# Performance work log

Hardware: AMD Instinct MI355X
Metric: run time of the kernel (lower is better)

Reference implementation:

```python
import jax, jax.numpy as jnp
import numpy as np
from jax import lax

B, S, H, W = 64, 256, 512, 512


def _lstm_cell(x_t, h, c, Wih, Whh, bih, bhh):
    # PyTorch LSTMCell gate order: i, f, g, o
    g = x_t @ Wih.T + h @ Whh.T + bih + bhh  # [B, 4H]
    i, f, gg, o = jnp.split(g, 4, axis=-1)
    c_new = jax.nn.sigmoid(f) * c + jax.nn.sigmoid(i) * jnp.tanh(gg)
    h_new = jax.nn.sigmoid(o) * jnp.tanh(c_new)
    return h_new, c_new


def setup_inputs() -> dict:
    key = jax.random.key(0)
    ks = jax.random.split(key, 12)
    bnd = 1.0 / np.sqrt(H)
    u = lambda k, shape, b: jax.random.uniform(k, shape, jnp.float32, -b, b)
    return {
        "x": jax.random.normal(ks[0], (B, S, S), jnp.float32),
        "enc_Wih": u(ks[1], (4 * H, S), bnd),
        "enc_Whh": u(ks[2], (4 * H, H), bnd),
        "enc_bih": u(ks[3], (4 * H,), bnd),
        "enc_bhh": u(ks[4], (4 * H,), bnd),
        "dec_Wih": u(ks[5], (4 * H, S), bnd),
        "dec_Whh": u(ks[6], (4 * H, H), bnd),
        "dec_bih": u(ks[7], (4 * H,), bnd),
        "dec_bhh": u(ks[8], (4 * H,), bnd),
        "w1": u(ks[9], (W, H), 1.0 / np.sqrt(H)),
        "w2": u(ks[10], (W, H), 1.0 / np.sqrt(H)),
        "vt": u(ks[11], (W,), 1.0 / np.sqrt(W)),
    }


def reference(x, enc_Wih, enc_Whh, enc_bih, enc_bhh,
              dec_Wih, dec_Whh, dec_bih, dec_bhh, w1, w2, vt):
    xs = x.transpose(1, 0, 2)  # [S, B, S] time-major

    # ---- encoder LSTM (zero initial state, PyTorch default) ----
    def enc_step(carry, x_t):
        h, c = carry
        h, c = _lstm_cell(x_t, h, c, enc_Wih, enc_Whh, enc_bih, enc_bhh)
        return (h, c), h

    h0 = jnp.zeros((B, H), x.dtype)
    (hT, cT), enc_out = lax.scan(enc_step, (h0, h0), xs)  # enc_out: [S, B, H]

    # loop-invariant W1 projection of encoder outputs
    e1 = jnp.einsum('sbh,wh->sbw', enc_out, w1)  # [S, B, W]

    # ---- decoder: hidden updates each step; cell stays at cT (faithful to source) ----
    def dec_step(h, x_t):
        h_new, _ = _lstm_cell(x_t, h, cT, dec_Wih, dec_Whh, dec_bih, dec_bhh)
        att = jnp.tanh(e1 + (h_new @ w2.T)[None, :, :])   # [S, B, W]
        scores = jnp.einsum('sbw,w->sb', att, vt)          # [S, B]
        lp = jax.nn.log_softmax(scores.T, axis=-1)         # [B, S]
        return h_new, lp

    _, probs = lax.scan(dec_step, hT, xs)  # [S_dec, B, S]
    return probs.transpose(1, 0, 2)        # [B, S_dec, S]
```

## Files before the change

kernel.cpp:

```cpp
#include <hip/hip_runtime.h>
#include <cmath>

__device__ __forceinline__ float sigm(float x) { return 1.0f / (1.0f + __expf(-x)); }

__global__ __launch_bounds__(256) void transpose_w(const float* __restrict__ in,
                                                   float* __restrict__ outT, int K) {
  __shared__ float tile[32][33];
  int tx = threadIdx.x & 31, ty = threadIdx.x >> 5;
  int k0 = blockIdx.x * 32;
  int j0 = blockIdx.y * 32;
#pragma unroll
  for (int i = 0; i < 32; i += 8)
    tile[ty + i][tx] = in[(size_t)(j0 + ty + i) * K + k0 + tx];
  __syncthreads();
#pragma unroll
  for (int i = 0; i < 32; i += 8)
    outT[(size_t)(k0 + ty + i) * 2048 + j0 + tx] = tile[tx][ty + i];
}

__device__ __forceinline__ void gemv_j(const float4* __restrict__ A4,
                                       const float4* __restrict__ W4, int j, int kqx,
                                       int kq, int jlo, int jhi, int b0, int b1,
                                       float (&o0)[8], float (&o1)[8]) {
  int qa = (j << 3) + kqx;
  float4 a04 = A4[b0 * 192 + qa];
  float4 a14 = A4[b1 * 192 + qa];
  int wr = ((j << 3) + kq) << 2;
  float a0v[4] = {a04.x, a04.y, a04.z, a04.w};
  float a1v[4] = {a14.x, a14.y, a14.z, a14.w};
#pragma unroll
  for (int i = 0; i < 4; ++i) {
    float4 wlo = W4[(wr + i) * 8 + jlo];
    float4 whi = W4[(wr + i) * 8 + jhi];
    o0[0] = fmaf(a0v[i], wlo.x, o0[0]);
    o0[1] = fmaf(a0v[i], wlo.y, o0[1]);
    o0[2] = fmaf(a0v[i], wlo.z, o0[2]);
    o0[3] = fmaf(a0v[i], wlo.w, o0[3]);
    o0[4] = fmaf(a0v[i], whi.x, o0[4]);
    o0[5] = fmaf(a0v[i], whi.y, o0[5]);
    o0[6] = fmaf(a0v[i], whi.z, o0[6]);
    o0[7] = fmaf(a0v[i], whi.w, o0[7]);
    o1[0] = fmaf(a1v[i], wlo.x, o1[0]);
    o1[1] = fmaf(a1v[i], wlo.y, o1[1]);
    o1[2] = fmaf(a1v[i], wlo.z, o1[2]);
    o1[3] = fmaf(a1v[i], wlo.w, o1[3]);
    o1[4] = fmaf(a1v[i], whi.x, o1[4]);
    o1[5] = fmaf(a1v[i], whi.y, o1[5]);
    o1[6] = fmaf(a1v[i], whi.z, o1[6]);
    o1[7] = fmaf(a1v[i], whi.w, o1[7]);
  }
}

__global__ __launch_bounds__(256, 1) void lstm_chain(
    const float* __restrict__ WT, const float* __restrict__ x,
    const float* __restrict__ bih, const float* __restrict__ bhh,
    float* __restrict__ HBUF,
    float* __restrict__ Cst,
    unsigned int* __restrict__ flg,
    int is_enc) {
  extern __shared__ float lds[];
  float4* W4 = (float4*)lds;
  float4* A4 = (float4*)(lds + 24576);
  float* gates = lds + 24576 + 12288;
  const int bg = blockIdx.x >> 6, ng = blockIdx.x & 63;
  const int tid = threadIdx.x;
  unsigned int* myflag = flg + (size_t)(bg * 64 + ng) * 32;
  unsigned int* dom = flg + (size_t)bg * 64 * 32;

#pragma unroll
  for (int r = 0; r < 24; ++r) {
    int idx = tid + 256 * r;
    int k = idx >> 3, j = idx & 7;
    float4 v =
        *(const float4*)(WT + (size_t)k * 2048 + (j >> 1) * 512 + ng * 8 + (j & 1) * 4);
    W4[k * 8 + (j ^ ((k >> 2) & 7))] = v;
  }
  float bi_i = 0.f, bi_f = 0.f, bi_g = 0.f, bi_o = 0.f, creg = 0.f;
  if (tid < 128) {
    int b = tid >> 3, n8 = tid & 7;
    int n_g = ng * 8 + n8;
    bi_i = bih[n_g] + bhh[n_g];
    bi_f = bih[512 + n_g] + bhh[512 + n_g];
    bi_g = bih[1024 + n_g] + bhh[1024 + n_g];
    bi_o = bih[1536 + n_g] + bhh[1536 + n_g];
    if (!is_enc) creg = Cst[(size_t)(bg * 16 + b) * 512 + n_g];
  }
#pragma unroll
  for (int r = 0; r < 8; ++r) {
    int idx = tid + 256 * r;
    int b = idx >> 7, q = idx & 127;
    float4 v;
    if (is_enc)
      v = make_float4(0.f, 0.f, 0.f, 0.f);
    else
      v = *(const float4*)(HBUF + ((size_t)(255 * 64) + bg * 16 + b) * 512 + 4 * q);
    A4[b * 192 + (q ^ ((b >> 1) & 7))] = v;
  }
#pragma unroll
  for (int r = 0; r < 4; ++r) {
    int idx = tid + 256 * r;
    int b = idx >> 6, q = idx & 63;
    float4 v = *(const float4*)(x + ((size_t)(bg * 16 + b) * 256 + 0) * 256 + 4 * q);
    A4[b * 192 + ((128 + q) ^ ((b >> 1) & 7))] = v;
  }
  __syncthreads();

  const int w = tid >> 6;
  const int lane = tid & 63;
  const int kq = lane >> 3, b8 = lane & 7;
  const int b0 = 2 * b8, b1 = b0 + 1;
  const int jlo = (2 * w) ^ kq, jhi = (2 * w + 1) ^ kq;
  const int kqx = kq ^ b8;

  for (int t = 0; t < 256; ++t) {
    float acc0[8], acc1[8];
#pragma unroll
    for (int g = 0; g < 8; ++g) { acc0[g] = 0.f; acc1[g] = 0.f; }
#pragma unroll 2
    for (int j = 0; j < 24; ++j)
      gemv_j(A4, W4, j, kqx, kq, jlo, jhi, b0, b1, acc0, acc1);
#pragma unroll
    for (int d = 8; d <= 32; d <<= 1) {
#pragma unroll
      for (int g = 0; g < 8; ++g) {
        acc0[g] += __shfl_xor(acc0[g], d, 64);
        acc1[g] += __shfl_xor(acc1[g], d, 64);
      }
    }
    if (kq == 0) {
#pragma unroll
      for (int g = 0; g < 8; ++g) {
        gates[b0 * 40 + w * 8 + g] = acc0[g];
        gates[b1 * 40 + w * 8 + g] = acc1[g];
      }
    }
    __syncthreads();
    if (tid < 128) {
      int b = tid >> 3, n8 = tid & 7;
      float pi = gates[b * 40 + n8] + bi_i;
      float pf = gates[b * 40 + 8 + n8] + bi_f;
      float pg = gates[b * 40 + 16 + n8] + bi_g;
      float po = gates[b * 40 + 24 + n8] + bi_o;
      float ig = sigm(pi), fg = sigm(pf), gg = tanhf(pg), og = sigm(po);
      float cn = fmaf(fg, creg, ig * gg);
      if (is_enc) creg = cn;
      float hn = og * tanhf(cn);
      float* hp = HBUF + ((size_t)t * 64 + bg * 16 + b) * 512 + ng * 8 + n8;
      __hip_atomic_store(hp, hn, __ATOMIC_RELAXED, __HIP_MEMORY_SCOPE_AGENT);
      if (is_enc && t == 255) Cst[(size_t)(bg * 16 + b) * 512 + ng * 8 + n8] = cn;
    }
    if (t == 255) break;
    asm volatile("s_waitcnt vmcnt(0)" ::: "memory");
    __syncthreads();
    if (tid == 0)
      __hip_atomic_store(myflag, (unsigned)(t + 1), __ATOMIC_RELAXED,
                         __HIP_MEMORY_SCOPE_AGENT);
    asm volatile("" ::: "memory");
#pragma unroll
    for (int r = 0; r < 4; ++r) {
      int idx = tid + 256 * r;
      int b = idx >> 6, q = idx & 63;
      float4 v =
          *(const float4*)(x + ((size_t)(bg * 16 + b) * 256 + (t + 1)) * 256 + 4 * q);
      A4[b * 192 + ((128 + q) ^ ((b >> 1) & 7))] = v;
    }
    if (tid < 64) {
      const unsigned tgt = (unsigned)(t + 1);
      unsigned int* fp = dom + (size_t)tid * 32;
      while (true) {
        unsigned v = __hip_atomic_load(fp, __ATOMIC_RELAXED, __HIP_MEMORY_SCOPE_AGENT);
        if (__all((int)(v >= tgt))) break;
        __builtin_amdgcn_s_sleep(1);
      }
    }
    __syncthreads();
    const float4* hb = (const float4*)(HBUF + (size_t)t * 64 * 512);
#pragma unroll
    for (int r = 0; r < 8; ++r) {
      int idx = tid + 256 * r;
      int b = idx >> 7, q = idx & 127;
      float4 v = hb[(size_t)(bg * 16 + b) * 128 + q];
      A4[b * 192 + (q ^ ((b >> 1) & 7))] = v;
    }
    __syncthreads();
  }
}

__global__ __launch_bounds__(256) void gemm_fp32(const float* __restrict__ A,
                                                 const float* __restrict__ W,
                                                 float* __restrict__ C, int N, int K) {
  __shared__ float As[16 * 132];
  __shared__ float Ws[16 * 132];
  int tid = threadIdx.x;
  int n0 = blockIdx.x * 128, m0 = blockIdx.y * 128;
  int row = tid >> 1;
  int kbase = (tid & 1) * 8;
  const float* ap = A + (size_t)(m0 + row) * K;
  const float* wp = W + (size_t)(n0 + row) * K;
  int ty = tid >> 4, tx = tid & 15;
  float acc[8][8];
#pragma unroll
  for (int i = 0; i < 8; ++i)
#pragma unroll
    for (int j = 0; j < 8; ++j) acc[i][j] = 0.f;

  for (int kt = 0; kt < K; kt += 16) {
    float4 va0 = *(const float4*)(ap + kt + kbase);
    float4 va1 = *(const float4*)(ap + kt + kbase + 4);
    float4 vw0 = *(const float4*)(wp + kt + kbase);
    float4 vw1 = *(const float4*)(wp + kt + kbase + 4);
    __syncthreads();
    As[(kbase + 0) * 132 + row] = va0.x;
    As[(kbase + 1) * 132 + row] = va0.y;
    As[(kbase + 2) * 132 + row] = va0.z;
    As[(kbase + 3) * 132 + row] = va0.w;
    As[(kbase + 4) * 132 + row] = va1.x;
    As[(kbase + 5) * 132 + row] = va1.y;
    As[(kbase + 6) * 132 + row] = va1.z;
    As[(kbase + 7) * 132 + row] = va1.w;
    Ws[(kbase + 0) * 132 + row] = vw0.x;
    Ws[(kbase + 1) * 132 + row] = vw0.y;
    Ws[(kbase + 2) * 132 + row] = vw0.z;
    Ws[(kbase + 3) * 132 + row] = vw0.w;
    Ws[(kbase + 4) * 132 + row] = vw1.x;
    Ws[(kbase + 5) * 132 + row] = vw1.y;
    Ws[(kbase + 6) * 132 + row] = vw1.z;
    Ws[(kbase + 7) * 132 + row] = vw1.w;
    __syncthreads();
#pragma unroll
    for (int kk = 0; kk < 16; ++kk) {
      float4 a0 = *(const float4*)&As[kk * 132 + ty * 8];
      float4 a1 = *(const float4*)&As[kk * 132 + ty * 8 + 4];
      float4 w0 = *(const float4*)&Ws[kk * 132 + tx * 8];
      float4 w1 = *(const float4*)&Ws[kk * 132 + tx * 8 + 4];
      float av[8] = {a0.x, a0.y, a0.z, a0.w, a1.x, a1.y, a1.z, a1.w};
      float wv[8] = {w0.x, w0.y, w0.z, w0.w, w1.x, w1.y, w1.z, w1.w};
#pragma unroll
      for (int i = 0; i < 8; ++i)
#pragma unroll
        for (int j = 0; j < 8; ++j) acc[i][j] = fmaf(av[i], wv[j], acc[i][j]);
    }
  }
#pragma unroll
  for (int i = 0; i < 8; ++i) {
    float* cp = C + (size_t)(m0 + ty * 8 + i) * N + n0 + tx * 8;
    *(float4*)cp = make_float4(acc[i][0], acc[i][1], acc[i][2], acc[i][3]);
    *(float4*)(cp + 4) = make_float4(acc[i][4], acc[i][5], acc[i][6], acc[i][7]);
  }
}

__global__ __launch_bounds__(256) void scorer(const float* __restrict__ E1,
                                              const float* __restrict__ H2,
                                              const float* __restrict__ vt,
                                              float* __restrict__ out) {
  extern __shared__ float smem[];
  float* e1s = smem;
  float* h2s = smem + 8256;
  int tid = threadIdx.x;
  int sx = blockIdx.x;
  int b = blockIdx.y;
#pragma unroll
  for (int j = 0; j < 8; ++j) {
    int idx = tid + 256 * j;
    int r = idx >> 7, c4 = idx & 127;
    float4 v = *(const float4*)(E1 + ((size_t)(sx * 16 + r) * 64 + b) * 512 + c4 * 4);
    *(float4*)&e1s[r * 516 + c4 * 4] = v;
  }
  int tl = tid >> 4, sl = tid & 15;
  for (int tt = 0; tt < 16; ++tt) {
    __syncthreads();
#pragma unroll
    for (int j = 0; j < 8; ++j) {
      int idx = tid + 256 * j;
      int r = idx >> 7, c4 = idx & 127;
      float4 v = *(const float4*)(H2 + ((size_t)(tt * 16 + r) * 64 + b) * 512 + c4 * 4);
      *(float4*)&h2s[r * 516 + c4 * 4] = v;
    }
    __syncthreads();
    float acc = 0.f;
    const float* ep = &e1s[sl * 516];
    const float* hp = &h2s[tl * 516];
#pragma unroll 8
    for (int w4 = 0; w4 < 128; ++w4) {
      float4 a = *(const float4*)(ep + w4 * 4);
      float4 h = *(const float4*)(hp + w4 * 4);
      float4 vv = *(const float4*)(vt + w4 * 4);
      float x0 = a.x + h.x, x1 = a.y + h.y, x2 = a.z + h.z, x3 = a.w + h.w;
      float t0 = fmaf(-2.f, __builtin_amdgcn_rcpf(__expf(x0 + x0) + 1.f), 1.f);
      float t1 = fmaf(-2.f, __builtin_amdgcn_rcpf(__expf(x1 + x1) + 1.f), 1.f);
      float t2 = fmaf(-2.f, __builtin_amdgcn_rcpf(__expf(x2 + x2) + 1.f), 1.f);
      float t3 = fmaf(-2.f, __builtin_amdgcn_rcpf(__expf(x3 + x3) + 1.f), 1.f);
      acc = fmaf(t0, vv.x, acc);
      acc = fmaf(t1, vv.y, acc);
      acc = fmaf(t2, vv.z, acc);
      acc = fmaf(t3, vv.w, acc);
    }
    out[((size_t)b * 256 + tt * 16 + tl) * 256 + sx * 16 + sl] = acc;
  }
}

__global__ __launch_bounds__(256) void logsoftmax_kernel(float* __restrict__ out) {
  __shared__ float red[256];
  int tid = threadIdx.x;
  float* row = out + (size_t)blockIdx.x * 256;
  float v = row[tid];
  red[tid] = v;
  __syncthreads();
  for (int off = 128; off > 0; off >>= 1) {
    if (tid < off) red[tid] = fmaxf(red[tid], red[tid + off]);
    __syncthreads();
  }
  float mx = red[0];
  __syncthreads();
  red[tid] = __expf(v - mx);
  __syncthreads();
  for (int off = 128; off > 0; off >>= 1) {
    if (tid < off) red[tid] += red[tid + off];
    __syncthreads();
  }
  float lse = logf(red[0]);
  row[tid] = v - mx - lse;
}

extern "C" void kernel_launch(void* const* d_in, const int* in_sizes, int n_in,
                              void* d_out, int out_size, void* d_ws, size_t ws_size,
                              hipStream_t stream) {
  (void)in_sizes; (void)n_in; (void)out_size; (void)ws_size;
  const float* x = (const float*)d_in[0];
  const float* eWih = (const float*)d_in[1];
  const float* eWhh = (const float*)d_in[2];
  const float* ebih = (const float*)d_in[3];
  const float* ebhh = (const float*)d_in[4];
  const float* dWih = (const float*)d_in[5];
  const float* dWhh = (const float*)d_in[6];
  const float* dbih = (const float*)d_in[7];
  const float* dbhh = (const float*)d_in[8];
  const float* w1 = (const float*)d_in[9];
  const float* w2 = (const float*)d_in[10];
  const float* vt = (const float*)d_in[11];
  float* out = (float*)d_out;
  float* ws = (float*)d_ws;

  float* E1 = ws;
  float* H2 = E1 + 8388608ull;
  float* HBUF = H2 + 8388608ull;
  float* WTe = HBUF + 8388608ull;
  float* WTd = WTe + 1572864ull;
  float* Cst = WTd + 1572864ull;
  unsigned int* FLG = (unsigned int*)(Cst + 32768ull);

  const unsigned ldsB = (24576 + 12288 + 640) * 4;
  const unsigned scorerLds = 2 * 16 * 516 * 4;

  hipMemsetAsync(FLG, 0, 16384 * sizeof(unsigned int), stream);
  transpose_w<<<dim3(16, 64), 256, 0, stream>>>(eWhh, WTe, 512);
  transpose_w<<<dim3(8, 64), 256, 0, stream>>>(eWih, WTe + 512 * 2048, 256);
  transpose_w<<<dim3(16, 64), 256, 0, stream>>>(dWhh, WTd, 512);
  transpose_w<<<dim3(8, 64), 256, 0, stream>>>(dWih, WTd + 512 * 2048, 256);

  {
    const float* a0 = WTe; const float* a1 = x; const float* a2 = ebih;
    const float* a3 = ebhh; float* a4 = HBUF; float* a5 = Cst;
    unsigned int* a6 = FLG; int a7 = 1;
    void* args[] = {&a0, &a1, &a2, &a3, &a4, &a5, &a6, &a7};
    hipLaunchCooperativeKernel((const void*)lstm_chain, dim3(256), dim3(256), args,
                               ldsB, stream);
  }
  gemm_fp32<<<dim3(4, 128), 256, 0, stream>>>(HBUF, w1, E1, 512, 512);
  {
    const float* a0 = WTd; const float* a1 = x; const float* a2 = dbih;
    const float* a3 = dbhh; float* a4 = HBUF; float* a5 = Cst;
    unsigned int* a6 = FLG + 8192; int a7 = 0;
    void* args[] = {&a0, &a1, &a2, &a3, &a4, &a5, &a6, &a7};
    hipLaunchCooperativeKernel((const void*)lstm_chain, dim3(256), dim3(256), args,
                               ldsB, stream);
  }
  gemm_fp32<<<dim3(4, 128), 256, 0, stream>>>(HBUF, w2, H2, 512, 512);
  scorer<<<dim3(16, 64), 256, scorerLds, stream>>>(E1, H2, vt, out);
  logsoftmax_kernel<<<16384, 256, 0, stream>>>(out);
}
```

Before: 4.029 ms.

## Double LSTM block threads, split flag signaling, and spread scorer over time chunks

The recurrent LSTM kernel now runs 512 threads per block, with each wavefront computing one gate for 8 batch rows, which halves the per-thread serial GEMV work in each step. The block-wide barrier before polling is replaced: two wavefronts each publish their own flag, one wavefront polls the peer flags and then releases the others through an LDS variable, so the whole block no longer waits on a barrier before polling. The scorer grid gains a z dimension so each block handles 2 time tiles instead of 16, giving more parallelism at the cost of reloading E1 in every block. Risks are the more intricate synchronisation protocol and higher register and occupancy pressure.

```diff
diff --git a/kernel.cpp b/kernel.cpp
--- a/kernel.cpp
+++ b/kernel.cpp
@@ -18,40 +18,7 @@
     outT[(size_t)(k0 + ty + i) * 2048 + j0 + tx] = tile[tx][ty + i];
 }
 
-__device__ __forceinline__ void gemv_j(const float4* __restrict__ A4,
-                                       const float4* __restrict__ W4, int j, int kqx,
-                                       int kq, int jlo, int jhi, int b0, int b1,
-                                       float (&o0)[8], float (&o1)[8]) {
-  int qa = (j << 3) + kqx;
-  float4 a04 = A4[b0 * 192 + qa];
-  float4 a14 = A4[b1 * 192 + qa];
-  int wr = ((j << 3) + kq) << 2;
-  float a0v[4] = {a04.x, a04.y, a04.z, a04.w};
-  float a1v[4] = {a14.x, a14.y, a14.z, a14.w};
-#pragma unroll
-  for (int i = 0; i < 4; ++i) {
-    float4 wlo = W4[(wr + i) * 8 + jlo];
-    float4 whi = W4[(wr + i) * 8 + jhi];
-    o0[0] = fmaf(a0v[i], wlo.x, o0[0]);
-    o0[1] = fmaf(a0v[i], wlo.y, o0[1]);
-    o0[2] = fmaf(a0v[i], wlo.z, o0[2]);
-    o0[3] = fmaf(a0v[i], wlo.w, o0[3]);
-    o0[4] = fmaf(a0v[i], whi.x, o0[4]);
-    o0[5] = fmaf(a0v[i], whi.y, o0[5]);
-    o0[6] = fmaf(a0v[i], whi.z, o0[6]);
-    o0[7] = fmaf(a0v[i], whi.w, o0[7]);
-    o1[0] = fmaf(a1v[i], wlo.x, o1[0]);
-    o1[1] = fmaf(a1v[i], wlo.y, o1[1]);
-    o1[2] = fmaf(a1v[i], wlo.z, o1[2]);
-    o1[3] = fmaf(a1v[i], wlo.w, o1[3]);
-    o1[4] = fmaf(a1v[i], whi.x, o1[4]);
-    o1[5] = fmaf(a1v[i], whi.y, o1[5]);
-    o1[6] = fmaf(a1v[i], whi.z, o1[6]);
-    o1[7] = fmaf(a1v[i], whi.w, o1[7]);
-  }
-}
-
-__global__ __launch_bounds__(256, 1) void lstm_chain(
+__global__ __launch_bounds__(512, 1) void lstm_chain(
     const float* __restrict__ WT, const float* __restrict__ x,
     const float* __restrict__ bih, const float* __restrict__ bhh,
     float* __restrict__ HBUF,
@@ -62,14 +29,16 @@
   float4* W4 = (float4*)lds;
   float4* A4 = (float4*)(lds + 24576);
   float* gates = lds + 24576 + 12288;
+  unsigned int* ldsrel = (unsigned int*)(lds + 24576 + 12288 + 640);
   const int bg = blockIdx.x >> 6, ng = blockIdx.x & 63;
   const int tid = threadIdx.x;
-  unsigned int* myflag = flg + (size_t)(bg * 64 + ng) * 32;
-  unsigned int* dom = flg + (size_t)bg * 64 * 32;
-
-#pragma unroll
-  for (int r = 0; r < 24; ++r) {
-    int idx = tid + 256 * r;
+  unsigned int* fl0 = flg + ((size_t)(bg * 64 + ng) * 2 + 0) * 32;
+  unsigned int* dmn = flg + (size_t)bg * 4096;
+  if (tid == 0) *ldsrel = 0u;
+
+#pragma unroll
+  for (int r = 0; r < 12; ++r) {
+    int idx = tid + 512 * r;
     int k = idx >> 3, j = idx & 7;
     float4 v =
         *(const float4*)(WT + (size_t)k * 2048 + (j >> 1) * 512 + ng * 8 + (j & 1) * 4);
@@ -86,8 +55,8 @@
     if (!is_enc) creg = Cst[(size_t)(bg * 16 + b) * 512 + n_g];
   }
 #pragma unroll
-  for (int r = 0; r < 8; ++r) {
-    int idx = tid + 256 * r;
+  for (int r = 0; r < 4; ++r) {
+    int idx = tid + 512 * r;
     int b = idx >> 7, q = idx & 127;
     float4 v;
     if (is_enc)
@@ -97,90 +66,109 @@
     A4[b * 192 + (q ^ ((b >> 1) & 7))] = v;
   }
 #pragma unroll
-  for (int r = 0; r < 4; ++r) {
-    int idx = tid + 256 * r;
+  for (int r = 0; r < 2; ++r) {
+    int idx = tid + 512 * r;
     int b = idx >> 6, q = idx & 63;
     float4 v = *(const float4*)(x + ((size_t)(bg * 16 + b) * 256 + 0) * 256 + 4 * q);
     A4[b * 192 + ((128 + q) ^ ((b >> 1) & 7))] = v;
   }
   __syncthreads();
 
-  const int w = tid >> 6;
+  const int w8 = tid >> 6;
+  const int gate = w8 & 3, bh = w8 >> 2;
   const int lane = tid & 63;
   const int kq = lane >> 3, b8 = lane & 7;
-  const int b0 = 2 * b8, b1 = b0 + 1;
-  const int jlo = (2 * w) ^ kq, jhi = (2 * w + 1) ^ kq;
-  const int kqx = kq ^ b8;
+  const int b = bh * 8 + b8;
+  const int sb = (b >> 1) & 7;
+  const int jlo = (2 * gate) ^ kq, jhi = jlo ^ 1;
 
   for (int t = 0; t < 256; ++t) {
-    float acc0[8], acc1[8];
-#pragma unroll
-    for (int g = 0; g < 8; ++g) { acc0[g] = 0.f; acc1[g] = 0.f; }
+    float acc[8];
+#pragma unroll
+    for (int g = 0; g < 8; ++g) acc[g] = 0.f;
 #pragma unroll 2
-    for (int j = 0; j < 24; ++j)
-      gemv_j(A4, W4, j, kqx, kq, jlo, jhi, b0, b1, acc0, acc1);
+    for (int j = 0; j < 24; ++j) {
+      float4 av = A4[b * 192 + (j << 3) + (kq ^ sb)];
+      float a0v[4] = {av.x, av.y, av.z, av.w};
+      int wr = ((j << 3) + kq) << 2;
+#pragma unroll
+      for (int i = 0; i < 4; ++i) {
+        float4 wlo = W4[(wr + i) * 8 + jlo];
+        float4 whi = W4[(wr + i) * 8 + jhi];
+        acc[0] = fmaf(a0v[i], wlo.x, acc[0]);
+        acc[1] = fmaf(a0v[i], wlo.y, acc[1]);
+        acc[2] = fmaf(a0v[i], wlo.z, acc[2]);
+        acc[3] = fmaf(a0v[i], wlo.w, acc[3]);
+        acc[4] = fmaf(a0v[i], whi.x, acc[4]);
+        acc[5] = fmaf(a0v[i], whi.y, acc[5]);
+        acc[6] = fmaf(a0v[i], whi.z, acc[6]);
+        acc[7] = fmaf(a0v[i], whi.w, acc[7]);
+      }
+    }
 #pragma unroll
     for (int d = 8; d <= 32; d <<= 1) {
 #pragma unroll
-      for (int g = 0; g < 8; ++g) {
-        acc0[g] += __shfl_xor(acc0[g], d, 64);
-        acc1[g] += __shfl_xor(acc1[g], d, 64);
-      }
+      for (int g = 0; g < 8; ++g) acc[g] += __shfl_xor(acc[g], d, 64);
     }
     if (kq == 0) {
 #pragma unroll
-      for (int g = 0; g < 8; ++g) {
-        gates[b0 * 40 + w * 8 + g] = acc0[g];
-        gates[b1 * 40 + w * 8 + g] = acc1[g];
-      }
+      for (int g = 0; g < 8; ++g) gates[b * 40 + gate * 8 + g] = acc[g];
     }
     __syncthreads();
     if (tid < 128) {
-      int b = tid >> 3, n8 = tid & 7;
-      float pi = gates[b * 40 + n8] + bi_i;
-      float pf = gates[b * 40 + 8 + n8] + bi_f;
-      float pg = gates[b * 40 + 16 + n8] + bi_g;
-      float po = gates[b * 40 + 24 + n8] + bi_o;
+      int bb = tid >> 3, n8 = tid & 7;
+      float pi = gates[bb * 40 + n8] + bi_i;
+      float pf = gates[bb * 40 + 8 + n8] + bi_f;
+      float pg = gates[bb * 40 + 16 + n8] + bi_g;
+      float po = gates[bb * 40 + 24 + n8] + bi_o;
       float ig = sigm(pi), fg = sigm(pf), gg = tanhf(pg), og = sigm(po);
       float cn = fmaf(fg, creg, ig * gg);
       if (is_enc) creg = cn;
       float hn = og * tanhf(cn);
-      float* hp = HBUF + ((size_t)t * 64 + bg * 16 + b) * 512 + ng * 8 + n8;
+      float* hp = HBUF + ((size_t)t * 64 + bg * 16 + bb) * 512 + ng * 8 + n8;
       __hip_atomic_store(hp, hn, __ATOMIC_RELAXED, __HIP_MEMORY_SCOPE_AGENT);
-      if (is_enc && t == 255) Cst[(size_t)(bg * 16 + b) * 512 + ng * 8 + n8] = cn;
+      if (is_enc && t == 255) Cst[(size_t)(bg * 16 + bb) * 512 + ng * 8 + n8] = cn;
     }
     if (t == 255) break;
-    asm volatile("s_waitcnt vmcnt(0)" ::: "memory");
-    __syncthreads();
-    if (tid == 0)
-      __hip_atomic_store(myflag, (unsigned)(t + 1), __ATOMIC_RELAXED,
-                         __HIP_MEMORY_SCOPE_AGENT);
-    asm volatile("" ::: "memory");
-#pragma unroll
-    for (int r = 0; r < 4; ++r) {
-      int idx = tid + 256 * r;
-      int b = idx >> 6, q = idx & 63;
+    if (w8 < 2) {
+      asm volatile("s_waitcnt vmcnt(0)" ::: "memory");
+      if (lane == 0)
+        __hip_atomic_store(fl0 + w8 * 32, (unsigned)(t + 1), __ATOMIC_RELAXED,
+                           __HIP_MEMORY_SCOPE_AGENT);
+      asm volatile("" ::: "memory");
+    }
+#pragma unroll
+    for (int r = 0; r < 2; ++r) {
+      int idx = tid + 512 * r;
+      int bb = idx >> 6, q = idx & 63;
       float4 v =
-          *(const float4*)(x + ((size_t)(bg * 16 + b) * 256 + (t + 1)) * 256 + 4 * q);
-      A4[b * 192 + ((128 + q) ^ ((b >> 1) & 7))] = v;
-    }
-    if (tid < 64) {
-      const unsigned tgt = (unsigned)(t + 1);
-      unsigned int* fp = dom + (size_t)tid * 32;
+          *(const float4*)(x + ((size_t)(bg * 16 + bb) * 256 + (t + 1)) * 256 + 4 * q);
+      A4[bb * 192 + ((128 + q) ^ ((bb >> 1) & 7))] = v;
+    }
+    const unsigned tgt = (unsigned)(t + 1);
+    if (w8 == 7) {
+      unsigned int* fp0 = dmn + (size_t)lane * 64;
       while (true) {
-        unsigned v = __hip_atomic_load(fp, __ATOMIC_RELAXED, __HIP_MEMORY_SCOPE_AGENT);
-        if (__all((int)(v >= tgt))) break;
+        unsigned v0 = __hip_atomic_load(fp0, __ATOMIC_RELAXED, __HIP_MEMORY_SCOPE_AGENT);
+        unsigned v1 =
+            __hip_atomic_load(fp0 + 32, __ATOMIC_RELAXED, __HIP_MEMORY_SCOPE_AGENT);
+        if (__all((int)(v0 >= tgt && v1 >= tgt))) break;
         __builtin_amdgcn_s_sleep(1);
       }
-    }
-    __syncthreads();
+      if (lane == 0)
+        __hip_atomic_store(ldsrel, tgt, __ATOMIC_RELEASE, __HIP_MEMORY_SCOPE_WORKGROUP);
+    } else {
+      while (__hip_atomic_load(ldsrel, __ATOMIC_ACQUIRE, __HIP_MEMORY_SCOPE_WORKGROUP) <
+             tgt)
+        __builtin_amdgcn_s_sleep(1);
+    }
     const float4* hb = (const float4*)(HBUF + (size_t)t * 64 * 512);
 #pragma unroll
-    for (int r = 0; r < 8; ++r) {
-      int idx = tid + 256 * r;
-      int b = idx >> 7, q = idx & 127;
-      float4 v = hb[(size_t)(bg * 16 + b) * 128 + q];
-      A4[b * 192 + (q ^ ((b >> 1) & 7))] = v;
+    for (int r = 0; r < 4; ++r) {
+      int idx = tid + 512 * r;
+      int bb = idx >> 7, q = idx & 127;
+      float4 v = hb[(size_t)(bg * 16 + bb) * 128 + q];
+      A4[bb * 192 + (q ^ ((bb >> 1) & 7))] = v;
     }
     __syncthreads();
   }
@@ -259,6 +247,7 @@
   int tid = threadIdx.x;
   int sx = blockIdx.x;
   int b = blockIdx.y;
+  int tz = blockIdx.z;
 #pragma unroll
   for (int j = 0; j < 8; ++j) {
     int idx = tid + 256 * j;
@@ -267,7 +256,8 @@
     *(float4*)&e1s[r * 516 + c4 * 4] = v;
   }
   int tl = tid >> 4, sl = tid & 15;
-  for (int tt = 0; tt < 16; ++tt) {
+  for (int tu = 0; tu < 2; ++tu) {
+    int tt = tz * 2 + tu;
     __syncthreads();
 #pragma unroll
     for (int j = 0; j < 8; ++j) {
@@ -349,10 +339,10 @@
   float* Cst = WTd + 1572864ull;
   unsigned int* FLG = (unsigned int*)(Cst + 32768ull);
 
-  const unsigned ldsB = (24576 + 12288 + 640) * 4;
+  const unsigned ldsB = (24576 + 12288 + 640 + 16) * 4;
   const unsigned scorerLds = 2 * 16 * 516 * 4;
 
-  hipMemsetAsync(FLG, 0, 16384 * sizeof(unsigned int), stream);
+  hipMemsetAsync(FLG, 0, 32768 * sizeof(unsigned int), stream);
   transpose_w<<<dim3(16, 64), 256, 0, stream>>>(eWhh, WTe, 512);
   transpose_w<<<dim3(8, 64), 256, 0, stream>>>(eWih, WTe + 512 * 2048, 256);
   transpose_w<<<dim3(16, 64), 256, 0, stream>>>(dWhh, WTd, 512);
@@ -363,19 +353,19 @@
     const float* a3 = ebhh; float* a4 = HBUF; float* a5 = Cst;
     unsigned int* a6 = FLG; int a7 = 1;
     void* args[] = {&a0, &a1, &a2, &a3, &a4, &a5, &a6, &a7};
-    hipLaunchCooperativeKernel((const void*)lstm_chain, dim3(256), dim3(256), args,
+    hipLaunchCooperativeKernel((const void*)lstm_chain, dim3(256), dim3(512), args,
                                ldsB, stream);
   }
   gemm_fp32<<<dim3(4, 128), 256, 0, stream>>>(HBUF, w1, E1, 512, 512);
   {
     const float* a0 = WTd; const float* a1 = x; const float* a2 = dbih;
     const float* a3 = dbhh; float* a4 = HBUF; float* a5 = Cst;
-    unsigned int* a6 = FLG + 8192; int a7 = 0;
+    unsigned int* a6 = FLG + 16384; int a7 = 0;
     void* args[] = {&a0, &a1, &a2, &a3, &a4, &a5, &a6, &a7};
-    hipLaunchCooperativeKernel((const void*)lstm_chain, dim3(256), dim3(256), args,
+    hipLaunchCooperativeKernel((const void*)lstm_chain, dim3(256), dim3(512), args,
                                ldsB, stream);
   }
   gemm_fp32<<<dim3(4, 128), 256, 0, stream>>>(HBUF, w2, H2, 512, 512);
-  scorer<<<dim3(16, 64), 256, scorerLds, stream>>>(E1, H2, vt, out);
+  scorer<<<dim3(16, 64, 8), 256, scorerLds, stream>>>(E1, H2, vt, out);
   logsoftmax_kernel<<<16384, 256, 0, stream>>>(out);
 }
```

After: 4.949 ms. 1.23x slower.

## Use per-wave flags and per-wave polling to cut LSTM step barriers; split scorer over time

Applied to the files above, without the earlier changes.

The LSTM step handshake now has each of the two gate-producing waves publish its own flag right after its stores drain, so the block-wide barrier before signalling goes away. Each wave then polls only the 32 producer flags whose hidden-state slice it will load, and copies just that slice into LDS. This should shorten the critical path of the 256 serial steps. Separately, the scorer grid gains a z dimension of 8 so each block handles 2 time tiles instead of 16, giving more parallelism at the cost of reloading the E1 tile 8 times.

```diff
diff --git a/kernel.cpp b/kernel.cpp
--- a/kernel.cpp
+++ b/kernel.cpp
@@ -64,8 +64,7 @@
   float* gates = lds + 24576 + 12288;
   const int bg = blockIdx.x >> 6, ng = blockIdx.x & 63;
   const int tid = threadIdx.x;
-  unsigned int* myflag = flg + (size_t)(bg * 64 + ng) * 32;
-  unsigned int* dom = flg + (size_t)bg * 64 * 32;
+  unsigned int* dom = flg + (size_t)bg * 4096;
 
 #pragma unroll
   for (int r = 0; r < 24; ++r) {
@@ -109,8 +108,10 @@
   const int lane = tid & 63;
   const int kq = lane >> 3, b8 = lane & 7;
   const int b0 = 2 * b8, b1 = b0 + 1;
-  const int jlo = (2 * w) ^ kq, jhi = (2 * w + 1) ^ kq;
+  const int jlo = (2 * w) ^ kq, jhi = jlo ^ 1;
   const int kqx = kq ^ b8;
+  const int rb = lane >> 2, rqg = lane & 3;
+  const int rsb = (rb >> 1) & 7;
 
   for (int t = 0; t < 256; ++t) {
     float acc0[8], acc1[8];
@@ -136,51 +137,58 @@
     }
     __syncthreads();
     if (tid < 128) {
-      int b = tid >> 3, n8 = tid & 7;
-      float pi = gates[b * 40 + n8] + bi_i;
-      float pf = gates[b * 40 + 8 + n8] + bi_f;
-      float pg = gates[b * 40 + 16 + n8] + bi_g;
-      float po = gates[b * 40 + 24 + n8] + bi_o;
+      int bb = tid >> 3, n8 = tid & 7;
+      float pi = gates[bb * 40 + n8] + bi_i;
+      float pf = gates[bb * 40 + 8 + n8] + bi_f;
+      float pg = gates[bb * 40 + 16 + n8] + bi_g;
+      float po = gates[bb * 40 + 24 + n8] + bi_o;
       float ig = sigm(pi), fg = sigm(pf), gg = tanhf(pg), og = sigm(po);
       float cn = fmaf(fg, creg, ig * gg);
       if (is_enc) creg = cn;
       float hn = og * tanhf(cn);
-      float* hp = HBUF + ((size_t)t * 64 + bg * 16 + b) * 512 + ng * 8 + n8;
+      float* hp = HBUF + ((size_t)t * 64 + bg * 16 + bb) * 512 + ng * 8 + n8;
       __hip_atomic_store(hp, hn, __ATOMIC_RELAXED, __HIP_MEMORY_SCOPE_AGENT);
-      if (is_enc && t == 255) Cst[(size_t)(bg * 16 + b) * 512 + ng * 8 + n8] = cn;
+      if (is_enc && t == 255) Cst[(size_t)(bg * 16 + bb) * 512 + ng * 8 + n8] = cn;
     }
     if (t == 255) break;
-    asm volatile("s_waitcnt vmcnt(0)" ::: "memory");
-    __syncthreads();
-    if (tid == 0)
-      __hip_atomic_store(myflag, (unsigned)(t + 1), __ATOMIC_RELAXED,
-                         __HIP_MEMORY_SCOPE_AGENT);
-    asm volatile("" ::: "memory");
+    const unsigned tgt = (unsigned)(t + 1);
+    if (w < 2) {
+      asm volatile("s_waitcnt vmcnt(0)" ::: "memory");
+      if (lane == 0)
+        __hip_atomic_store(dom + ((size_t)ng * 2 + w) * 32, tgt, __ATOMIC_RELAXED,
+                           __HIP_MEMORY_SCOPE_AGENT);
+      asm volatile("" ::: "memory");
+    }
 #pragma unroll
     for (int r = 0; r < 4; ++r) {
       int idx = tid + 256 * r;
-      int b = idx >> 6, q = idx & 63;
+      int bb = idx >> 6, q = idx & 63;
       float4 v =
-          *(const float4*)(x + ((size_t)(bg * 16 + b) * 256 + (t + 1)) * 256 + 4 * q);
-      A4[b * 192 + ((128 + q) ^ ((b >> 1) & 7))] = v;
-    }
-    if (tid < 64) {
-      const unsigned tgt = (unsigned)(t + 1);
-      unsigned int* fp = dom + (size_t)tid * 32;
-      while (true) {
-        unsigned v = __hip_atomic_load(fp, __ATOMIC_RELAXED, __HIP_MEMORY_SCOPE_AGENT);
-        if (__all((int)(v >= tgt))) break;
-        __builtin_amdgcn_s_sleep(1);
+          *(const float4*)(x + ((size_t)(bg * 16 + bb) * 256 + (t + 1)) * 256 + 4 * q);
+      A4[bb * 192 + ((128 + q) ^ ((bb >> 1) & 7))] = v;
+    }
+    {
+      int ok;
+      if (lane < 32) {
+        unsigned int* fp = dom + ((size_t)(w * 16 + (lane & 15)) * 2 + (lane >> 4)) * 32;
+        while (true) {
+          unsigned v = __hip_atomic_load(fp, __ATOMIC_RELAXED, __HIP_MEMORY_SCOPE_AGENT);
+          ok = (int)(v >= tgt);
+          if (__all(ok)) break;
+          __builtin_amdgcn_s_sleep(1);
+        }
+      } else {
+        while (!__all(1)) {}
       }
     }
-    __syncthreads();
-    const float4* hb = (const float4*)(HBUF + (size_t)t * 64 * 512);
-#pragma unroll
-    for (int r = 0; r < 8; ++r) {
-      int idx = tid + 256 * r;
-      int b = idx >> 7, q = idx & 127;
-      float4 v = hb[(size_t)(bg * 16 + b) * 128 + q];
-      A4[b * 192 + (q ^ ((b >> 1) & 7))] = v;
+    {
+      const float4* hb = (const float4*)(HBUF + (size_t)t * 64 * 512);
+#pragma unroll
+      for (int u = 0; u < 8; ++u) {
+        int q = w * 32 + rqg * 8 + u;
+        float4 v = hb[(size_t)(bg * 16 + rb) * 128 + q];
+        A4[rb * 192 + (q ^ rsb)] = v;
+      }
     }
     __syncthreads();
   }
@@ -259,6 +267,7 @@
   int tid = threadIdx.x;
   int sx = blockIdx.x;
   int b = blockIdx.y;
+  int tz = blockIdx.z;
 #pragma unroll
   for (int j = 0; j < 8; ++j) {
     int idx = tid + 256 * j;
@@ -267,7 +276,8 @@
     *(float4*)&e1s[r * 516 + c4 * 4] = v;
   }
   int tl = tid >> 4, sl = tid & 15;
-  for (int tt = 0; tt < 16; ++tt) {
+  for (int tu = 0; tu < 2; ++tu) {
+    int tt = tz * 2 + tu;
     __syncthreads();
 #pragma unroll
     for (int j = 0; j < 8; ++j) {
@@ -352,7 +362,7 @@
   const unsigned ldsB = (24576 + 12288 + 640) * 4;
   const unsigned scorerLds = 2 * 16 * 516 * 4;
 
-  hipMemsetAsync(FLG, 0, 16384 * sizeof(unsigned int), stream);
+  hipMemsetAsync(FLG, 0, 32768 * sizeof(unsigned int), stream);
   transpose_w<<<dim3(16, 64), 256, 0, stream>>>(eWhh, WTe, 512);
   transpose_w<<<dim3(8, 64), 256, 0, stream>>>(eWih, WTe + 512 * 2048, 256);
   transpose_w<<<dim3(16, 64), 256, 0, stream>>>(dWhh, WTd, 512);
@@ -370,12 +380,12 @@
   {
     const float* a0 = WTd; const float* a1 = x; const float* a2 = dbih;
     const float* a3 = dbhh; float* a4 = HBUF; float* a5 = Cst;
-    unsigned int* a6 = FLG + 8192; int a7 = 0;
+    unsigned int* a6 = FLG + 16384; int a7 = 0;
     void* args[] = {&a0, &a1, &a2, &a3, &a4, &a5, &a6, &a7};
     hipLaunchCooperativeKernel((const void*)lstm_chain, dim3(256), dim3(256), args,
                                ldsB, stream);
   }
   gemm_fp32<<<dim3(4, 128), 256, 0, stream>>>(HBUF, w2, H2, 512, 512);
-  scorer<<<dim3(16, 64), 256, scorerLds, stream>>>(E1, H2, vt, out);
+  scorer<<<dim3(16, 64, 8), 256, scorerLds, stream>>>(E1, H2, vt, out);
   logsoftmax_kernel<<<16384, 256, 0, stream>>>(out);
 }
```

Measured after the change: 4.626 ms. +14.8%, slower.
